# Kernel optimization log

Measured on AMD Instinct MI355X. Metric: run time of the kernel, lower is better.

The kernel has to match this reference:

```python
import jax, jax.numpy as jnp
import numpy as np

D_MODEL = 1024
N_HEADS = 16
D_HEAD = D_MODEL // N_HEADS
D_FF = 4096
ACT_BITS = 8
GSIZE = 64
EPS = 1e-6


def act_quant(x):
    # per-group int8 activation quantization with straight-through estimator
    qmax = 2.0 ** (ACT_BITS - 1) - 1.0  # 127
    g = x.reshape(x.shape[:-1] + (-1, GSIZE))
    s = jnp.clip(jnp.max(jnp.abs(g), axis=-1, keepdims=True), 1e-5, None) / qmax
    q = jnp.clip(jnp.round(g / s), -qmax, qmax) * s
    out = g + jax.lax.stop_gradient(q - g)  # STE
    return out.reshape(x.shape)


def weight_quant_1b(w):
    # binarize to sign(w) * mean(|w|), STE
    alpha = jnp.mean(jnp.abs(w))
    wq = jnp.sign(w) * alpha
    return w + jax.lax.stop_gradient(wq - w)


def bitlinear(x, w):
    # y = Q_act(x) @ Q_w(w)^T ; w is [out, in]
    return act_quant(x) @ weight_quant_1b(w).T


def rmsnorm(x, g):
    return x * jax.lax.rsqrt(jnp.mean(x * x, axis=-1, keepdims=True) + EPS) * g


def causal_sdpa(q, k, v):
    # q,k,v: [B,H,T,Dh]
    T = q.shape[2]
    scores = jnp.einsum('bhqd,bhkd->bhqk', q, k) / jnp.sqrt(jnp.asarray(D_HEAD, q.dtype))
    mask = jnp.tril(jnp.ones((T, T), dtype=bool))
    scores = jnp.where(mask, scores, jnp.asarray(-1e30, q.dtype))
    p = jax.nn.softmax(scores, axis=-1)
    return jnp.einsum('bhqk,bhkd->bhqd', p, v)


def setup_inputs() -> dict:
    key = jax.random.key(0)
    ks = jax.random.split(key, 11)
    sd = 0.02
    inp = {
        'x': jax.random.normal(ks[0], (1, 4096, D_MODEL), dtype=jnp.float32),
        'wq': jax.random.normal(ks[1], (D_MODEL, D_MODEL), dtype=jnp.float32) * sd,
        'wk': jax.random.normal(ks[2], (D_MODEL, D_MODEL), dtype=jnp.float32) * sd,
        'wv': jax.random.normal(ks[3], (D_MODEL, D_MODEL), dtype=jnp.float32) * sd,
        'wo': jax.random.normal(ks[4], (D_MODEL, D_MODEL), dtype=jnp.float32) * sd,
        'w1': jax.random.normal(ks[5], (D_FF, D_MODEL), dtype=jnp.float32) * sd,
        'w2': jax.random.normal(ks[6], (D_FF, D_MODEL), dtype=jnp.float32) * sd,
        'w3': jax.random.normal(ks[7], (D_MODEL, D_FF), dtype=jnp.float32) * sd,
        'g1': jnp.ones((D_MODEL,), dtype=jnp.float32),
        'g2': jnp.ones((D_MODEL,), dtype=jnp.float32),
    }
    return inp


def reference(x, wq, wk, wv, wo, w1, w2, w3, g1, g2):
    B, T, C = x.shape
    # attention branch
    h = rmsnorm(x, g1)
    q = bitlinear(h, wq).reshape(B, T, N_HEADS, D_HEAD).transpose(0, 2, 1, 3)
    k = bitlinear(h, wk).reshape(B, T, N_HEADS, D_HEAD).transpose(0, 2, 1, 3)
    v = bitlinear(h, wv).reshape(B, T, N_HEADS, D_HEAD).transpose(0, 2, 1, 3)
    y = causal_sdpa(q, k, v).transpose(0, 2, 1, 3).reshape(B, T, C)
    x = x + bitlinear(y, wo)
    # SwiGLU FFN branch
    h2 = rmsnorm(x, g2)
    ff = bitlinear(jax.nn.silu(bitlinear(h2, w1)) * bitlinear(h2, w2), w3)
    return x + ff
```

## Files before the change

kernel.cpp:

```cpp
#include <hip/hip_runtime.h>
#include <math.h>


typedef unsigned short u16;
typedef __attribute__((ext_vector_type(4))) float f32x4;
typedef __attribute__((ext_vector_type(4))) unsigned short u16x4;
typedef __attribute__((ext_vector_type(8))) unsigned short u16x8;
typedef __attribute__((ext_vector_type(8))) __bf16 bf16x8;

#define DEV static __device__ __forceinline__

DEV float bf2f(u16 u) { union { unsigned i; float f; } c; c.i = ((unsigned)u) << 16; return c.f; }
DEV u16 f2bf(float f) { __bf16 b = (__bf16)f; return __builtin_bit_cast(u16, b); }
DEV float fexp2(float x) { float r; asm("v_exp_f32 %0, %1" : "=v"(r) : "v"(x)); return r; }

DEV void gload16(const void* g, void* l) {
  __builtin_amdgcn_global_load_lds((__attribute__((address_space(1))) void*)g,
                                   (__attribute__((address_space(3))) void*)l,
                                   16, 0, 0);
}

__global__ __launch_bounds__(256) void convert_sign_all(
    const float* __restrict__ w0, const float* __restrict__ w1,
    const float* __restrict__ w2, const float* __restrict__ w3,
    const float* __restrict__ w4, const float* __restrict__ w5,
    const float* __restrict__ w6, u16* __restrict__ sgn_base,
    float* __restrict__ partial) {
  __shared__ float red[4];
  const int wi = blockIdx.y;
  const float* srcs[7] = {w0, w1, w2, w3, w4, w5, w6};
  const size_t offs[7] = {0, 1048576, 2097152, 3145728, 4194304, 4194304, 12582912};
  const float* w = srcs[wi];
  u16* sgn = sgn_base + offs[wi];
  const int n4 = (wi < 4) ? 262144 : 1048576;
  const bool ilv = (wi == 4) || (wi == 5);
  const int ilv_add = (wi == 5) ? 16 : 0;

  float s = 0.f;
  for (int i = blockIdx.x * 256 + threadIdx.x; i < n4; i += 256 * 256) {
    f32x4 v = ((const f32x4*)w)[i];
    u16x4 o;
#pragma unroll
    for (int j = 0; j < 4; ++j) {
      float f = v[j];
      o[j] = f > 0.f ? (u16)0x3F80 : (f < 0.f ? (u16)0xBF80 : (u16)0);
      s += fabsf(f);
    }
    size_t di = i;
    if (ilv) {
      int e = i << 2;
      int row = e >> 10, col = e & 1023;
      int dst = ((row >> 4) << 5) + ilv_add + (row & 15);
      di = ((size_t)dst << 8) + (col >> 2);
    }
    ((u16x4*)sgn)[di] = o;
  }
#pragma unroll
  for (int off = 32; off >= 1; off >>= 1) s += __shfl_xor(s, off);
  if ((threadIdx.x & 63) == 0) red[threadIdx.x >> 6] = s;
  __syncthreads();
  if (threadIdx.x == 0)
    partial[wi * 256 + blockIdx.x] = red[0] + red[1] + red[2] + red[3];
}

__global__ __launch_bounds__(256) void finalize_alpha(
    const float* __restrict__ partial, float* __restrict__ alphas) {
  __shared__ float red[4];
  int wi = blockIdx.x;
  float v = partial[wi * 256 + threadIdx.x];
#pragma unroll
  for (int off = 32; off >= 1; off >>= 1) v += __shfl_xor(v, off);
  if ((threadIdx.x & 63) == 0) red[threadIdx.x >> 6] = v;
  __syncthreads();
  if (threadIdx.x == 0)
    alphas[wi] = (red[0] + red[1] + red[2] + red[3]) *
                 (wi < 4 ? (1.f / 1048576.f) : (1.f / 4194304.f));
}

__global__ __launch_bounds__(256) void rmsnorm_quant(
    const float* __restrict__ x, const float* __restrict__ g, u16* __restrict__ out) {
  __shared__ float red[4];
  const int row = blockIdx.x, t = threadIdx.x;
  f32x4 v = ((const f32x4*)(x + (size_t)row * 1024))[t];
  float ss = v[0] * v[0] + v[1] * v[1] + v[2] * v[2] + v[3] * v[3];
#pragma unroll
  for (int off = 32; off >= 1; off >>= 1) ss += __shfl_xor(ss, off);
  if ((t & 63) == 0) red[t >> 6] = ss;
  __syncthreads();
  float tot = red[0] + red[1] + red[2] + red[3];
  float rinv = rsqrtf(tot * (1.f / 1024.f) + 1e-6f);
  f32x4 gg = ((const f32x4*)g)[t];
  float n[4];
#pragma unroll
  for (int j = 0; j < 4; ++j) n[j] = v[j] * rinv * gg[j];
  float gm = fmaxf(fmaxf(fabsf(n[0]), fabsf(n[1])), fmaxf(fabsf(n[2]), fabsf(n[3])));
#pragma unroll
  for (int off = 1; off <= 8; off <<= 1) gm = fmaxf(gm, __shfl_xor(gm, off));
  float s = fmaxf(gm, 1e-5f) / 127.0f;
  u16x4 o;
#pragma unroll
  for (int j = 0; j < 4; ++j) {
    float q = fminf(fmaxf(rintf(n[j] / s), -127.f), 127.f) * s;
    o[j] = f2bf(q);
  }
  ((u16x4*)out)[(size_t)row * 256 + t] = o;
}

__global__ __launch_bounds__(256) void transpose_v(
    const u16* __restrict__ qkv, u16* __restrict__ Vt) {
  __shared__ u16 T[64][65];
  const int tt = blockIdx.x, h = blockIdx.y, tid = threadIdx.x;
#pragma unroll
  for (int i = 0; i < 2; ++i) {
    int idx = i * 2048 + tid * 8;
    int trow = idx >> 6, dcol = idx & 63;
    u16x8 v = *(const u16x8*)(qkv + (size_t)(tt * 64 + trow) * 3072 + 2048 + h * 64 + dcol);
#pragma unroll
    for (int j = 0; j < 8; ++j) T[dcol + j][trow] = v[j];
  }
  __syncthreads();
#pragma unroll
  for (int i = 0; i < 2; ++i) {
    int idx = i * 2048 + tid * 8;
    int drow = idx >> 6, tcol = idx & 63;
    u16x8 v;
#pragma unroll
    for (int j = 0; j < 8; ++j) v[j] = T[drow][tcol + j];
    *(u16x8*)(Vt + ((size_t)h * 64 + drow) * 4096 + tt * 64 + tcol) = v;
  }
}

template <bool RES, int BM>
__global__ __launch_bounds__(256) void gemm_bt(
    const u16* __restrict__ A, const u16* __restrict__ B,
    const float* __restrict__ alpha, int ashift, const float* __restrict__ res,
    void* __restrict__ Cout, int M, int N, int K) {
  constexpr int NI = (BM == 128) ? 4 : 2;
  constexpr int WNE = (BM == 128) ? 64 : 32;
  __shared__ u16 As[BM * 64];
  __shared__ u16 Bs[128 * 64];
  const int tid = threadIdx.x;
  const int l = tid & 63, w = tid >> 6;
  const int wm = (BM == 128) ? (w >> 1) : 0;
  const int wn = (BM == 128) ? (w & 1) : w;
  const int lr = l & 15, lg = l >> 4;
  const int xorv = (l & 7) << 4;
  const int brow = blockIdx.y * BM;
  const int bcol = blockIdx.x * 128;
  const int src_chunk = (l & 7) ^ (l >> 3);
  const int rl = w * 8 + (l >> 3);

  f32x4 acc[4][NI];
#pragma unroll
  for (int i = 0; i < 4; ++i)
#pragma unroll
    for (int j = 0; j < NI; ++j) acc[i][j] = (f32x4){0.f, 0.f, 0.f, 0.f};

  const char* Ag = (const char*)A;
  const char* Bg = (const char*)B;
  const int nkt = K >> 6;
  for (int kt = 0; kt < nkt; ++kt) {
    __syncthreads();
    const size_t kb = (size_t)kt * 128 + src_chunk * 16;
#pragma unroll
    for (int it = 0; it < BM / 32; ++it)
      gload16(Ag + (size_t)(brow + it * 32 + rl) * (size_t)(K * 2) + kb,
              &As[(it * 32 + w * 8) * 64]);
#pragma unroll
    for (int it = 0; it < 4; ++it)
      gload16(Bg + (size_t)(bcol + it * 32 + rl) * (size_t)(K * 2) + kb,
              &Bs[(it * 32 + w * 8) * 64]);
    __syncthreads();

    bf16x8 af[4][2], bfr[NI][2];
#pragma unroll
    for (int mi = 0; mi < 4; ++mi)
#pragma unroll
      for (int ks = 0; ks < 2; ++ks) {
        int row = wm * 64 + mi * 16 + lr;
        af[mi][ks] = *(const bf16x8*)((const char*)As + row * 128 + ((ks * 64 + lg * 16) ^ xorv));
      }
#pragma unroll
    for (int ni = 0; ni < NI; ++ni)
#pragma unroll
      for (int ks = 0; ks < 2; ++ks) {
        int row = wn * WNE + ni * 16 + lr;
        bfr[ni][ks] = *(const bf16x8*)((const char*)Bs + row * 128 + ((ks * 64 + lg * 16) ^ xorv));
      }
#pragma unroll
    for (int ks = 0; ks < 2; ++ks)
#pragma unroll
      for (int mi = 0; mi < 4; ++mi)
#pragma unroll
        for (int ni = 0; ni < NI; ++ni)
          acc[mi][ni] = __builtin_amdgcn_mfma_f32_16x16x32_bf16(
              af[mi][ks], bfr[ni][ks], acc[mi][ni], 0, 0, 0);
  }

  const float scale = alpha[bcol >> ashift];
#pragma unroll
  for (int mi = 0; mi < 4; ++mi)
#pragma unroll
    for (int ni = 0; ni < NI; ++ni)
#pragma unroll
      for (int r = 0; r < 4; ++r) {
        int row = brow + wm * 64 + mi * 16 + lg * 4 + r;
        int col = bcol + wn * WNE + ni * 16 + lr;
        float vv = acc[mi][ni][r] * scale;
        if (RES)
          ((float*)Cout)[(size_t)row * N + col] = res[(size_t)row * N + col] + vv;
        else
          ((u16*)Cout)[(size_t)row * N + col] = f2bf(vv);
      }
}

__global__ __launch_bounds__(256) void gemm_ffn(
    const u16* __restrict__ A, const u16* __restrict__ B12,
    const float* __restrict__ alpha2, u16* __restrict__ zq) {
  __shared__ u16 As[128 * 64];
  __shared__ u16 Bs[128 * 64];
  const int tid = threadIdx.x;
  const int l = tid & 63, w = tid >> 6;
  const int wm = w >> 1, wn = w & 1;
  const int lr = l & 15, lg = l >> 4;
  const int xorv = (l & 7) << 4;
  const int brow = blockIdx.y * 128;
  const int bcol = blockIdx.x * 128;
  const int src_chunk = (l & 7) ^ (l >> 3);
  const int rl = w * 8 + (l >> 3);

  f32x4 acc[4][4];
#pragma unroll
  for (int i = 0; i < 4; ++i)
#pragma unroll
    for (int j = 0; j < 4; ++j) acc[i][j] = (f32x4){0.f, 0.f, 0.f, 0.f};

  for (int kt = 0; kt < 16; ++kt) {
    __syncthreads();
    const size_t kb = (size_t)kt * 128 + src_chunk * 16;
#pragma unroll
    for (int it = 0; it < 4; ++it) {
      gload16((const char*)A + (size_t)(brow + it * 32 + rl) * 2048 + kb,
              &As[(it * 32 + w * 8) * 64]);
      gload16((const char*)B12 + (size_t)(bcol + it * 32 + rl) * 2048 + kb,
              &Bs[(it * 32 + w * 8) * 64]);
    }
    __syncthreads();

    bf16x8 af[4][2], bfr[4][2];
#pragma unroll
    for (int mi = 0; mi < 4; ++mi)
#pragma unroll
      for (int ks = 0; ks < 2; ++ks) {
        int row = wm * 64 + mi * 16 + lr;
        af[mi][ks] = *(const bf16x8*)((const char*)As + row * 128 + ((ks * 64 + lg * 16) ^ xorv));
      }
#pragma unroll
    for (int ni = 0; ni < 4; ++ni)
#pragma unroll
      for (int ks = 0; ks < 2; ++ks) {
        int row = wn * 64 + ni * 16 + lr;
        bfr[ni][ks] = *(const bf16x8*)((const char*)Bs + row * 128 + ((ks * 64 + lg * 16) ^ xorv));
      }
#pragma unroll
    for (int ks = 0; ks < 2; ++ks)
#pragma unroll
      for (int mi = 0; mi < 4; ++mi)
#pragma unroll
        for (int ni = 0; ni < 4; ++ni)
          acc[mi][ni] = __builtin_amdgcn_mfma_f32_16x16x32_bf16(
              af[mi][ks], bfr[ni][ks], acc[mi][ni], 0, 0, 0);
  }

  const float a1 = alpha2[0], a2 = alpha2[1];
  const float L2E = 1.4426950408889634f;
  float zl[4][4], zh[4][4], rm[4][4];
#pragma unroll
  for (int mi = 0; mi < 4; ++mi)
#pragma unroll
    for (int r = 0; r < 4; ++r) {
      float y1 = acc[mi][0][r] * a1;
      zl[mi][r] = y1 / (1.f + fexp2(-L2E * y1)) * (acc[mi][1][r] * a2);
      float y3 = acc[mi][2][r] * a1;
      zh[mi][r] = y3 / (1.f + fexp2(-L2E * y3)) * (acc[mi][3][r] * a2);
      float g = fmaxf(fabsf(zl[mi][r]), fabsf(zh[mi][r]));
#pragma unroll
      for (int off = 1; off <= 8; off <<= 1) g = fmaxf(g, __shfl_xor(g, off));
      rm[mi][r] = g;
    }

  float* rmax = (float*)&As[0];
  __syncthreads();
  if (lr == 0) {
#pragma unroll
    for (int mi = 0; mi < 4; ++mi)
#pragma unroll
      for (int r = 0; r < 4; ++r)
        rmax[w * 64 + mi * 16 + lg * 4 + r] = rm[mi][r];
  }
  __syncthreads();

#pragma unroll
  for (int mi = 0; mi < 4; ++mi)
#pragma unroll
    for (int r = 0; r < 4; ++r) {
      float g = fmaxf(rm[mi][r], rmax[(w ^ 1) * 64 + mi * 16 + lg * 4 + r]);
      float gmc = fmaxf(g, 1e-5f);
      float s = gmc * (1.f / 127.f);
      float inv = 127.f / gmc;
      int row = brow + wm * 64 + mi * 16 + lg * 4 + r;
      int zc = blockIdx.x * 64 + wn * 32 + lr;
      float q0 = fminf(fmaxf(rintf(zl[mi][r] * inv), -127.f), 127.f) * s;
      float q1 = fminf(fmaxf(rintf(zh[mi][r] * inv), -127.f), 127.f) * s;
      zq[(size_t)row * 4096 + zc] = f2bf(q0);
      zq[(size_t)row * 4096 + zc + 16] = f2bf(q1);
    }
}

__global__ __launch_bounds__(256) void attn_kernel(
    const u16* __restrict__ QKV, const u16* __restrict__ Vt, u16* __restrict__ Y) {
  __shared__ u16 Ks[2][64 * 64];
  __shared__ u16 Vs[2][64 * 64];
  __shared__ u16 Ps[4][16 * 64];

  const int tid = threadIdx.x;
  const int l = tid & 63, w = tid >> 6;
  const int lr = l & 15, lg = l >> 4;
  const int xorv = (l & 7) << 4;
  const int h = blockIdx.x;
  const int y = blockIdx.y;
  const int qt = (y < 32) ? y : (95 - y);
  const int src_chunk = (l & 7) ^ (l >> 3);
  const int rl = w * 8 + (l >> 3);
  const float SC = 0.18033688f;

  const int qrow0 = qt * 64 + w * 16;
  const int nkt = qt + 1;

  bf16x8 qf[2];
#pragma unroll
  for (int ks = 0; ks < 2; ++ks)
    qf[ks] = __builtin_bit_cast(
        bf16x8, *(const u16x8*)(QKV + (size_t)(qrow0 + lr) * 3072 +
                                h * 64 + ks * 32 + lg * 8));

  f32x4 O[4];
#pragma unroll
  for (int ni = 0; ni < 4; ++ni) O[ni] = (f32x4){0.f, 0.f, 0.f, 0.f};
  float m_ = -3e38f, lsum = 0.f;

  auto STAGE = [&](int buf, int kt) {
#pragma unroll
    for (int it = 0; it < 2; ++it) {
      int krow = kt * 64 + it * 32 + rl;
      gload16((const char*)QKV + ((size_t)krow * 3072 + 1024 + h * 64) * 2 + src_chunk * 16,
              &Ks[buf][(it * 32 + w * 8) * 64]);
      int drow = it * 32 + rl;
      gload16((const char*)Vt + (((size_t)h * 64 + drow) * 4096 + kt * 64) * 2 + src_chunk * 16,
              &Vs[buf][(it * 32 + w * 8) * 64]);
    }
  };

  STAGE(0, 0);
#pragma unroll 1
  for (int kt = 0; kt < nkt; ++kt) {
    const int cur = kt & 1;
    if (kt + 1 < nkt) {
      STAGE(cur ^ 1, kt + 1);
      asm volatile("s_waitcnt vmcnt(4)" ::: "memory");
    } else {
      asm volatile("s_waitcnt vmcnt(0)" ::: "memory");
    }
    __builtin_amdgcn_s_barrier();
    __builtin_amdgcn_sched_barrier(0);

    const char* kbase = (const char*)&Ks[cur][0];
    const char* vbase = (const char*)&Vs[cur][0];

    f32x4 S[4];
    __builtin_amdgcn_s_setprio(1);
#pragma unroll
    for (int ni = 0; ni < 4; ++ni) {
      S[ni] = (f32x4){0.f, 0.f, 0.f, 0.f};
#pragma unroll
      for (int ks = 0; ks < 2; ++ks) {
        bf16x8 kf = *(const bf16x8*)(kbase + (ni * 16 + lr) * 128 +
                                     ((ks * 64 + lg * 16) ^ xorv));
        S[ni] = __builtin_amdgcn_mfma_f32_16x16x32_bf16(kf, qf[ks], S[ni], 0, 0, 0);
      }
    }
    __builtin_amdgcn_s_setprio(0);

#pragma unroll
    for (int ni = 0; ni < 4; ++ni)
#pragma unroll
      for (int r = 0; r < 4; ++r) S[ni][r] *= SC;
    if (kt == qt) {
#pragma unroll
      for (int ni = 0; ni < 4; ++ni)
#pragma unroll
        for (int r = 0; r < 4; ++r)
          if ((ni * 16 + lg * 4 + r) > (w * 16 + lr)) S[ni][r] = -3e38f;
    }

    float nm = -3e38f;
#pragma unroll
    for (int ni = 0; ni < 4; ++ni)
#pragma unroll
      for (int r = 0; r < 4; ++r) nm = fmaxf(nm, S[ni][r]);
    nm = fmaxf(nm, __shfl_xor(nm, 16));
    nm = fmaxf(nm, __shfl_xor(nm, 32));
    if (__ballot(nm > m_ + 8.f)) {
      float mn = fmaxf(m_, nm);
      float fac = fexp2(m_ - mn);
      m_ = mn;
      lsum *= fac;
#pragma unroll
      for (int ni = 0; ni < 4; ++ni) O[ni] *= fac;
    }
    float rs = 0.f;
#pragma unroll
    for (int ni = 0; ni < 4; ++ni)
#pragma unroll
      for (int r = 0; r < 4; ++r) {
        float pv = fexp2(S[ni][r] - m_);
        S[ni][r] = pv;
        rs += pv;
      }
    rs += __shfl_xor(rs, 16);
    rs += __shfl_xor(rs, 32);
    lsum += rs;

#pragma unroll
    for (int ni = 0; ni < 4; ++ni) {
      u16x4 pk;
#pragma unroll
      for (int r = 0; r < 4; ++r) pk[r] = f2bf(S[ni][r]);
      *(u16x4*)((char*)&Ps[w][0] + lr * 128 + ((ni * 32 + lg * 8) ^ xorv)) = pk;
    }
    bf16x8 pt[2];
#pragma unroll
    for (int ks = 0; ks < 2; ++ks)
      pt[ks] = *(const bf16x8*)((const char*)&Ps[w][0] + lr * 128 +
                                ((ks * 64 + lg * 16) ^ xorv));

    __builtin_amdgcn_s_setprio(1);
#pragma unroll
    for (int ni = 0; ni < 4; ++ni) {
#pragma unroll
      for (int ks = 0; ks < 2; ++ks) {
        bf16x8 vf = *(const bf16x8*)(vbase + (ni * 16 + lr) * 128 +
                                     ((ks * 64 + lg * 16) ^ xorv));
        O[ni] = __builtin_amdgcn_mfma_f32_16x16x32_bf16(vf, pt[ks], O[ni], 0, 0, 0);
      }
    }
    __builtin_amdgcn_s_setprio(0);
    asm volatile("" ::: "memory");
    __builtin_amdgcn_s_barrier();
  }

  float rinv = 1.f / lsum;
  float o[4][4];
  float gm = 0.f;
#pragma unroll
  for (int ni = 0; ni < 4; ++ni)
#pragma unroll
    for (int r = 0; r < 4; ++r) {
      o[ni][r] = O[ni][r] * rinv;
      gm = fmaxf(gm, fabsf(o[ni][r]));
    }
  gm = fmaxf(gm, __shfl_xor(gm, 16));
  gm = fmaxf(gm, __shfl_xor(gm, 32));
  float gmc = fmaxf(gm, 1e-5f);
  float s = gmc * (1.f / 127.f);
  float inv = 127.f / gmc;
#pragma unroll
  for (int ni = 0; ni < 4; ++ni) {
    u16x4 ov;
#pragma unroll
    for (int r = 0; r < 4; ++r) {
      float q = fminf(fmaxf(rintf(o[ni][r] * inv), -127.f), 127.f) * s;
      ov[r] = f2bf(q);
    }
    *(u16x4*)(Y + (size_t)(qrow0 + lr) * 1024 + h * 64 + ni * 16 + lg * 4) = ov;
  }
}

extern "C" void kernel_launch(void* const* d_in, const int* in_sizes, int n_in,
                              void* d_out, int out_size, void* d_ws, size_t ws_size,
                              hipStream_t stream) {
  const float* x  = (const float*)d_in[0];
  const float* wq = (const float*)d_in[1];
  const float* wk = (const float*)d_in[2];
  const float* wv = (const float*)d_in[3];
  const float* wo = (const float*)d_in[4];
  const float* w1 = (const float*)d_in[5];
  const float* w2 = (const float*)d_in[6];
  const float* w3 = (const float*)d_in[7];
  const float* g1 = (const float*)d_in[8];
  const float* g2 = (const float*)d_in[9];

  char* ws = (char*)d_ws;
  const size_t MB = 1024 * 1024;
  u16* sgn   = (u16*)ws;
  u16* sWq   = (u16*)(ws + 0 * MB);
  u16* sWo   = (u16*)(ws + 6 * MB);
  u16* sW12  = (u16*)(ws + 8 * MB);
  u16* sW3   = (u16*)(ws + 24 * MB);
  float* partial = (float*)(ws + 32 * MB);
  float* alphas  = (float*)(ws + 32 * MB + 16384);
  u16* Vt    = (u16*)(ws + 33 * MB);
  float* x1  = (float*)(ws + 33 * MB);
  u16* hq    = (u16*)(ws + 49 * MB);
  u16* qkv   = (u16*)(ws + 57 * MB);
  u16* yb    = (u16*)(ws + 81 * MB);
  u16* zq    = (u16*)(ws + 57 * MB);

  convert_sign_all<<<dim3(256, 7), 256, 0, stream>>>(wq, wk, wv, wo, w1, w2, w3,
                                                     sgn, partial);
  finalize_alpha<<<7, 256, 0, stream>>>(partial, alphas);

  rmsnorm_quant<<<4096, 256, 0, stream>>>(x, g1, hq);
  gemm_bt<false, 128><<<dim3(24, 32), 256, 0, stream>>>(hq, sWq, alphas, 10, nullptr,
                                                        qkv, 4096, 3072, 1024);
  transpose_v<<<dim3(64, 16), 256, 0, stream>>>(qkv, Vt);
  attn_kernel<<<dim3(16, 64), 256, 0, stream>>>(qkv, Vt, yb);
  gemm_bt<true, 64><<<dim3(8, 64), 256, 0, stream>>>(yb, sWo, alphas + 3, 31, x,
                                                     x1, 4096, 1024, 1024);
  rmsnorm_quant<<<4096, 256, 0, stream>>>(x1, g2, hq);
  gemm_ffn<<<dim3(64, 32), 256, 0, stream>>>(hq, sW12, alphas + 4, zq);
  gemm_bt<true, 64><<<dim3(8, 64), 256, 0, stream>>>(zq, sW3, alphas + 6, 31, x1,
                                                     (float*)d_out, 4096, 1024, 4096);
}
```

Before: 331.8 us.

## Fuse first RMSNorm into weight-sign kernel and enlarge FFN GEMM tile to 256 rows

The first rmsnorm+quant pass is folded into the weight sign-conversion launch as an extra blockIdx.y slice, which removes one kernel launch and lets that work overlap with weight conversion. Separately, the fused W1/W2 FFN GEMM now computes 256x128 tiles per block, each warp covering 128 rows, and A fragments are loaded per m-subtile inside the k loop. This raises reuse of the B tile and cuts the grid by half. In exchange it needs more accumulator registers and LDS, and fewer blocks are available to fill the GPU.

```diff
diff --git a/kernel.cpp b/kernel.cpp
--- a/kernel.cpp
+++ b/kernel.cpp
@@ -25,9 +25,45 @@
     const float* __restrict__ w2, const float* __restrict__ w3,
     const float* __restrict__ w4, const float* __restrict__ w5,
     const float* __restrict__ w6, u16* __restrict__ sgn_base,
-    float* __restrict__ partial) {
+    float* __restrict__ partial,
+    const float* __restrict__ x, const float* __restrict__ g1,
+    u16* __restrict__ hq) {
   __shared__ float red[4];
   const int wi = blockIdx.y;
+  const int t = threadIdx.x;
+
+  if (wi == 7) {
+#pragma unroll 1
+    for (int rr = 0; rr < 16; ++rr) {
+      const int row = blockIdx.x * 16 + rr;
+      f32x4 v = ((const f32x4*)(x + (size_t)row * 1024))[t];
+      float ss = v[0] * v[0] + v[1] * v[1] + v[2] * v[2] + v[3] * v[3];
+#pragma unroll
+      for (int off = 32; off >= 1; off >>= 1) ss += __shfl_xor(ss, off);
+      if ((t & 63) == 0) red[t >> 6] = ss;
+      __syncthreads();
+      float tot = red[0] + red[1] + red[2] + red[3];
+      __syncthreads();
+      float rinv = rsqrtf(tot * (1.f / 1024.f) + 1e-6f);
+      f32x4 gg = ((const f32x4*)g1)[t];
+      float n[4];
+#pragma unroll
+      for (int j = 0; j < 4; ++j) n[j] = v[j] * rinv * gg[j];
+      float gm = fmaxf(fmaxf(fabsf(n[0]), fabsf(n[1])), fmaxf(fabsf(n[2]), fabsf(n[3])));
+#pragma unroll
+      for (int off = 1; off <= 8; off <<= 1) gm = fmaxf(gm, __shfl_xor(gm, off));
+      float s = fmaxf(gm, 1e-5f) / 127.0f;
+      u16x4 o;
+#pragma unroll
+      for (int j = 0; j < 4; ++j) {
+        float q = fminf(fmaxf(rintf(n[j] / s), -127.f), 127.f) * s;
+        o[j] = f2bf(q);
+      }
+      ((u16x4*)hq)[(size_t)row * 256 + t] = o;
+    }
+    return;
+  }
+
   const float* srcs[7] = {w0, w1, w2, w3, w4, w5, w6};
   const size_t offs[7] = {0, 1048576, 2097152, 3145728, 4194304, 4194304, 12582912};
   const float* w = srcs[wi];
@@ -37,7 +73,7 @@
   const int ilv_add = (wi == 5) ? 16 : 0;
 
   float s = 0.f;
-  for (int i = blockIdx.x * 256 + threadIdx.x; i < n4; i += 256 * 256) {
+  for (int i = blockIdx.x * 256 + t; i < n4; i += 256 * 256) {
     f32x4 v = ((const f32x4*)w)[i];
     u16x4 o;
 #pragma unroll
@@ -57,9 +93,9 @@
   }
 #pragma unroll
   for (int off = 32; off >= 1; off >>= 1) s += __shfl_xor(s, off);
-  if ((threadIdx.x & 63) == 0) red[threadIdx.x >> 6] = s;
+  if ((t & 63) == 0) red[t >> 6] = s;
   __syncthreads();
-  if (threadIdx.x == 0)
+  if (t == 0)
     partial[wi * 256 + blockIdx.x] = red[0] + red[1] + red[2] + red[3];
 }
 
@@ -214,24 +250,24 @@
       }
 }
 
-__global__ __launch_bounds__(256) void gemm_ffn(
+__global__ __launch_bounds__(256, 2) void gemm_ffn(
     const u16* __restrict__ A, const u16* __restrict__ B12,
     const float* __restrict__ alpha2, u16* __restrict__ zq) {
-  __shared__ u16 As[128 * 64];
+  __shared__ u16 As[256 * 64];
   __shared__ u16 Bs[128 * 64];
   const int tid = threadIdx.x;
   const int l = tid & 63, w = tid >> 6;
   const int wm = w >> 1, wn = w & 1;
   const int lr = l & 15, lg = l >> 4;
   const int xorv = (l & 7) << 4;
-  const int brow = blockIdx.y * 128;
+  const int brow = blockIdx.y * 256;
   const int bcol = blockIdx.x * 128;
   const int src_chunk = (l & 7) ^ (l >> 3);
   const int rl = w * 8 + (l >> 3);
 
-  f32x4 acc[4][4];
-#pragma unroll
-  for (int i = 0; i < 4; ++i)
+  f32x4 acc[8][4];
+#pragma unroll
+  for (int i = 0; i < 8; ++i)
 #pragma unroll
     for (int j = 0; j < 4; ++j) acc[i][j] = (f32x4){0.f, 0.f, 0.f, 0.f};
 
@@ -239,44 +275,39 @@
     __syncthreads();
     const size_t kb = (size_t)kt * 128 + src_chunk * 16;
 #pragma unroll
-    for (int it = 0; it < 4; ++it) {
+    for (int it = 0; it < 8; ++it)
       gload16((const char*)A + (size_t)(brow + it * 32 + rl) * 2048 + kb,
               &As[(it * 32 + w * 8) * 64]);
+#pragma unroll
+    for (int it = 0; it < 4; ++it)
       gload16((const char*)B12 + (size_t)(bcol + it * 32 + rl) * 2048 + kb,
               &Bs[(it * 32 + w * 8) * 64]);
-    }
     __syncthreads();
 
-    bf16x8 af[4][2], bfr[4][2];
-#pragma unroll
-    for (int mi = 0; mi < 4; ++mi)
-#pragma unroll
-      for (int ks = 0; ks < 2; ++ks) {
-        int row = wm * 64 + mi * 16 + lr;
-        af[mi][ks] = *(const bf16x8*)((const char*)As + row * 128 + ((ks * 64 + lg * 16) ^ xorv));
-      }
-#pragma unroll
-    for (int ni = 0; ni < 4; ++ni)
-#pragma unroll
-      for (int ks = 0; ks < 2; ++ks) {
-        int row = wn * 64 + ni * 16 + lr;
-        bfr[ni][ks] = *(const bf16x8*)((const char*)Bs + row * 128 + ((ks * 64 + lg * 16) ^ xorv));
-      }
-#pragma unroll
-    for (int ks = 0; ks < 2; ++ks)
-#pragma unroll
-      for (int mi = 0; mi < 4; ++mi)
+#pragma unroll
+    for (int ks = 0; ks < 2; ++ks) {
+      bf16x8 bfr[4];
+#pragma unroll
+      for (int ni = 0; ni < 4; ++ni)
+        bfr[ni] = *(const bf16x8*)((const char*)Bs + (wn * 64 + ni * 16 + lr) * 128 +
+                                   ((ks * 64 + lg * 16) ^ xorv));
+#pragma unroll
+      for (int mi = 0; mi < 8; ++mi) {
+        bf16x8 af = *(const bf16x8*)((const char*)As + (wm * 128 + mi * 16 + lr) * 128 +
+                                     ((ks * 64 + lg * 16) ^ xorv));
 #pragma unroll
         for (int ni = 0; ni < 4; ++ni)
           acc[mi][ni] = __builtin_amdgcn_mfma_f32_16x16x32_bf16(
-              af[mi][ks], bfr[ni][ks], acc[mi][ni], 0, 0, 0);
+              af, bfr[ni], acc[mi][ni], 0, 0, 0);
+      }
+    }
   }
 
   const float a1 = alpha2[0], a2 = alpha2[1];
   const float L2E = 1.4426950408889634f;
-  float zl[4][4], zh[4][4], rm[4][4];
-#pragma unroll
-  for (int mi = 0; mi < 4; ++mi)
+  float zl[8][4], zh[8][4], rm[8][4];
+#pragma unroll
+  for (int mi = 0; mi < 8; ++mi)
 #pragma unroll
     for (int r = 0; r < 4; ++r) {
       float y1 = acc[mi][0][r] * a1;
@@ -293,22 +324,22 @@
   __syncthreads();
   if (lr == 0) {
 #pragma unroll
-    for (int mi = 0; mi < 4; ++mi)
+    for (int mi = 0; mi < 8; ++mi)
 #pragma unroll
       for (int r = 0; r < 4; ++r)
-        rmax[w * 64 + mi * 16 + lg * 4 + r] = rm[mi][r];
+        rmax[w * 128 + mi * 16 + lg * 4 + r] = rm[mi][r];
   }
   __syncthreads();
 
 #pragma unroll
-  for (int mi = 0; mi < 4; ++mi)
+  for (int mi = 0; mi < 8; ++mi)
 #pragma unroll
     for (int r = 0; r < 4; ++r) {
-      float g = fmaxf(rm[mi][r], rmax[(w ^ 1) * 64 + mi * 16 + lg * 4 + r]);
+      float g = fmaxf(rm[mi][r], rmax[(w ^ 1) * 128 + mi * 16 + lg * 4 + r]);
       float gmc = fmaxf(g, 1e-5f);
       float s = gmc * (1.f / 127.f);
       float inv = 127.f / gmc;
-      int row = brow + wm * 64 + mi * 16 + lg * 4 + r;
+      int row = brow + wm * 128 + mi * 16 + lg * 4 + r;
       int zc = blockIdx.x * 64 + wn * 32 + lr;
       float q0 = fminf(fmaxf(rintf(zl[mi][r] * inv), -127.f), 127.f) * s;
       float q1 = fminf(fmaxf(rintf(zh[mi][r] * inv), -127.f), 127.f) * s;
@@ -516,11 +547,10 @@
   u16* yb    = (u16*)(ws + 81 * MB);
   u16* zq    = (u16*)(ws + 57 * MB);
 
-  convert_sign_all<<<dim3(256, 7), 256, 0, stream>>>(wq, wk, wv, wo, w1, w2, w3,
-                                                     sgn, partial);
+  convert_sign_all<<<dim3(256, 8), 256, 0, stream>>>(wq, wk, wv, wo, w1, w2, w3,
+                                                     sgn, partial, x, g1, hq);
   finalize_alpha<<<7, 256, 0, stream>>>(partial, alphas);
 
-  rmsnorm_quant<<<4096, 256, 0, stream>>>(x, g1, hq);
   gemm_bt<false, 128><<<dim3(24, 32), 256, 0, stream>>>(hq, sWq, alphas, 10, nullptr,
                                                         qkv, 4096, 3072, 1024);
   transpose_v<<<dim3(64, 16), 256, 0, stream>>>(qkv, Vt);
@@ -528,7 +558,7 @@
   gemm_bt<true, 64><<<dim3(8, 64), 256, 0, stream>>>(yb, sWo, alphas + 3, 31, x,
                                                      x1, 4096, 1024, 1024);
   rmsnorm_quant<<<4096, 256, 0, stream>>>(x1, g2, hq);
-  gemm_ffn<<<dim3(64, 32), 256, 0, stream>>>(hq, sW12, alphas + 4, zq);
+  gemm_ffn<<<dim3(64, 16), 256, 0, stream>>>(hq, sW12, alphas + 4, zq);
   gemm_bt<true, 64><<<dim3(8, 64), 256, 0, stream>>>(zq, sW3, alphas + 6, 31, x1,
                                                      (float*)d_out, 4096, 1024, 4096);
 }
```

New measurement: 309.6 us. 1.07x faster.
